# Kernel optimization log

Measured on AMD Instinct MI355X. Metric: run time of the kernel, lower is better.

The kernel has to match this reference:

```python
import jax, jax.numpy as jnp
import numpy as np
import math

BS, NPOS, D_IN = 8, 384, 512
H, D_OUT = 8, 512
DK = D_OUT // H  # 64


def setup_inputs() -> dict:
    key = jax.random.key(0)
    ks = jax.random.split(key, 13)
    s = 0.02
    return {
        "q": jax.random.normal(ks[0], (BS, NPOS, D_IN), jnp.float32),
        "k": jax.random.normal(ks[1], (BS, NPOS, D_IN), jnp.float32),
        "v": jax.random.normal(ks[2], (BS, NPOS, D_IN), jnp.float32),
        "rpos_k": jax.random.normal(ks[3], (NPOS, NPOS, H, DK), jnp.float32) * s,
        "rpos_v": jax.random.normal(ks[4], (NPOS, NPOS, H, DK), jnp.float32) * s,
        "Wq": jax.random.normal(ks[5], (D_IN, D_OUT), jnp.float32) * s,
        "bq": jnp.zeros((D_OUT,), jnp.float32),
        "Wk": jax.random.normal(ks[6], (D_IN, D_OUT), jnp.float32) * s,
        "bk": jnp.zeros((D_OUT,), jnp.float32),
        "Wv": jax.random.normal(ks[7], (D_IN, D_OUT), jnp.float32) * s,
        "bv": jnp.zeros((D_OUT,), jnp.float32),
        "Wo": jax.random.normal(ks[8], (D_OUT, D_OUT), jnp.float32) * s,
        "bo": jnp.zeros((D_OUT,), jnp.float32),
    }


def reference(q, k, v, rpos_k, rpos_v, Wq, bq, Wk, bk, Wv, bv, Wo, bo):
    # model_name = 'with_pe' path; mask=None; dropout in eval mode (no-op)
    bs = q.shape[0]
    inv_sqrt_dk = 1.0 / math.sqrt(DK)

    qh = (q @ Wq + bq).reshape(bs, -1, H, DK).transpose(0, 2, 1, 3)  # bs,h,n,dk
    kh = (k @ Wk + bk).reshape(bs, -1, H, DK).transpose(0, 2, 1, 3)
    original_v = v @ Wv + bv                                          # bs,n,d_out
    vh = original_v.reshape(bs, -1, H, DK).transpose(0, 2, 1, 3)

    # standard content-content scores
    std_scores = jnp.einsum('bhnd,bhmd->bhnm', qh, kh) * inv_sqrt_dk
    # relative-position scores: q_n . rpos_k[n, m, h] -- computed inline,
    # no bs-broadcast materialization of rpos_k
    pos_scores = jnp.einsum('bhnd,nmhd->bhnm', qh, rpos_k) * inv_sqrt_dk

    scores = jax.nn.softmax(std_scores + pos_scores, axis=-1)
    # NOTE: original code divides the attention output by sqrt(d_k) again
    attn_out = jnp.einsum('bhnm,bhmd->bhnd', scores, vh) * inv_sqrt_dk

    concat = attn_out.transpose(0, 2, 1, 3).reshape(bs, -1, D_OUT)
    output = concat @ Wo + bo
    return (original_v, output)
```

## Files before the change

kernel.cpp:

```cpp
#include <hip/hip_runtime.h>

#define NPOS 384
#define DMODEL 512
#define NH 8
#define DK 64
#define BS 8
#define MROWS (BS * NPOS)
#define SROW (NPOS * NPOS)

typedef __attribute__((ext_vector_type(8))) short bf16x8;
typedef __attribute__((ext_vector_type(4))) float f32x4;

__device__ __forceinline__ unsigned short f2bf(float x) {
  unsigned int u = __float_as_uint(x);
  return (unsigned short)((u + 0x7fffu + ((u >> 16) & 1u)) >> 16);
}
__device__ __forceinline__ unsigned int pk2(float lo, float hi) {
  unsigned int ul = __float_as_uint(lo), uh = __float_as_uint(hi);
  ul = (ul + 0x7fffu + ((ul >> 16) & 1u)) >> 16;
  uh = (uh + 0x7fffu + ((uh >> 16) & 1u)) & 0xffff0000u;
  return ul | uh;
}
__device__ __forceinline__ bf16x8 pack8(float4 a, float4 b) {
  union { uint4 u; bf16x8 v; } cv;
  cv.u = make_uint4(pk2(a.x, a.y), pk2(a.z, a.w), pk2(b.x, b.y), pk2(b.z, b.w));
  return cv.v;
}

__global__ __launch_bounds__(256) void convert_all(
    const float* __restrict__ qin, const float* __restrict__ kin,
    const float* __restrict__ vin,
    const float* __restrict__ Wq, const float* __restrict__ Wk,
    const float* __restrict__ Wv, const float* __restrict__ Wo,
    unsigned short* __restrict__ qkvb, unsigned short* __restrict__ wt) {
  const int z = blockIdx.y;
  const int t = threadIdx.x;
  if (z < 3) {
    const float* src = z == 0 ? qin : z == 1 ? kin : vin;
    unsigned short* dst = qkvb + (size_t)z * MROWS * DMODEL;
    const size_t i = ((size_t)blockIdx.x * 256 + t) * 8;
    float4 a = *(const float4*)&src[i];
    float4 b = *(const float4*)&src[i + 4];
    union { uint4 u; bf16x8 v; } cv;
    cv.u = make_uint4(pk2(a.x, a.y), pk2(a.z, a.w), pk2(b.x, b.y), pk2(b.z, b.w));
    *(uint4*)&dst[i] = cv.u;
    return;
  }
  if (blockIdx.x >= 64) return;
  __shared__ float s[64][68];
  const int w = z - 3;
  const float* W = w == 0 ? Wq : w == 1 ? Wk : w == 2 ? Wv : Wo;
  unsigned short* out = wt + (size_t)w * DMODEL * DMODEL;
  const int k0 = (blockIdx.x & 7) * 64, n0 = (blockIdx.x >> 3) * 64;
#pragma unroll
  for (int i = 0; i < 4; ++i) {
    int f = t + i * 256;
    int kr = f >> 4, q4 = f & 15;
    *(float4*)&s[kr][q4 * 4] = *(const float4*)&W[(size_t)(k0 + kr) * DMODEL + n0 + q4 * 4];
  }
  __syncthreads();
#pragma unroll
  for (int i = 0; i < 2; ++i) {
    int slot = t + i * 256;
    int n = slot >> 3, kq = slot & 7;
    unsigned int p[4];
#pragma unroll
    for (int j = 0; j < 4; ++j)
      p[j] = pk2(s[kq * 8 + j * 2][n], s[kq * 8 + j * 2 + 1][n]);
    *(uint4*)&out[(size_t)(n0 + n) * DMODEL + k0 + kq * 8] = make_uint4(p[0], p[1], p[2], p[3]);
  }
}

__global__ __launch_bounds__(256) void proj_qkv(
    const unsigned short* __restrict__ qkvb,
    const unsigned short* __restrict__ wt,
    const float* __restrict__ bq, const float* __restrict__ bk, const float* __restrict__ bv,
    unsigned short* __restrict__ qhb, unsigned short* __restrict__ khb,
    float* __restrict__ origv, unsigned short* __restrict__ vhT) {
  __shared__ unsigned short As[64][72];
  __shared__ unsigned short Bs[64][72];
  const int z = blockIdx.z;
  const unsigned short* A = qkvb + (size_t)z * MROWS * DMODEL;
  const unsigned short* Wt = wt + (size_t)z * DMODEL * DMODEL;
  const float* bias = z == 0 ? bq : z == 1 ? bk : bv;
  const int m0 = blockIdx.x * 64, n0 = blockIdx.y * 64;
  const int t = threadIdx.x, lane = t & 63, w = t >> 6;
  const int wr = w >> 1, wc = w & 1;
  const int l15 = lane & 15, l4 = lane >> 4;
  f32x4 acc[2][2] = {};
  for (int kt = 0; kt < 8; ++kt) {
    const int k0 = kt * 64;
#pragma unroll
    for (int i = 0; i < 2; ++i) {
      int s = t + i * 256;
      int row = s >> 3, kq = s & 7;
      *(uint4*)&As[row][kq * 8] = *(const uint4*)&A[(size_t)(m0 + row) * DMODEL + k0 + kq * 8];
      *(uint4*)&Bs[row][kq * 8] = *(const uint4*)&Wt[(size_t)(n0 + row) * DMODEL + k0 + kq * 8];
    }
    __syncthreads();
    bf16x8 af[2][2], bfr[2][2];
#pragma unroll
    for (int mf = 0; mf < 2; ++mf)
#pragma unroll
      for (int ks = 0; ks < 2; ++ks)
        af[mf][ks] = *(const bf16x8*)&As[wr * 32 + mf * 16 + l15][ks * 32 + l4 * 8];
#pragma unroll
    for (int nf = 0; nf < 2; ++nf)
#pragma unroll
      for (int ks = 0; ks < 2; ++ks)
        bfr[nf][ks] = *(const bf16x8*)&Bs[wc * 32 + nf * 16 + l15][ks * 32 + l4 * 8];
#pragma unroll
    for (int mf = 0; mf < 2; ++mf)
#pragma unroll
      for (int nf = 0; nf < 2; ++nf)
#pragma unroll
        for (int ks = 0; ks < 2; ++ks)
          acc[mf][nf] = __builtin_amdgcn_mfma_f32_16x16x32_bf16(af[mf][ks], bfr[nf][ks],
                                                                acc[mf][nf], 0, 0, 0);
    __syncthreads();
  }
#pragma unroll
  for (int mf = 0; mf < 2; ++mf)
#pragma unroll
    for (int nf = 0; nf < 2; ++nf) {
      const int row0 = m0 + wr * 32 + mf * 16 + l4 * 4;
      const int col = n0 + wc * 32 + nf * 16 + l15;
      const float bi = bias[col];
      if (z == 0) {
#pragma unroll
        for (int i = 0; i < 4; ++i)
          qhb[(size_t)(row0 + i) * DMODEL + col] = f2bf((acc[mf][nf][i] + bi) * 0.125f);
      } else if (z == 1) {
#pragma unroll
        for (int i = 0; i < 4; ++i)
          khb[(size_t)(row0 + i) * DMODEL + col] = f2bf(acc[mf][nf][i] + bi);
      } else {
        const int b = row0 / NPOS, n = row0 - b * NPOS;
        const int h = col >> 6, d = col & 63;
        float vals[4];
#pragma unroll
        for (int i = 0; i < 4; ++i) {
          vals[i] = acc[mf][nf][i] + bi;
          origv[(size_t)(row0 + i) * DMODEL + col] = vals[i];
        }
        ushort4 pk;
        pk.x = f2bf(vals[0]); pk.y = f2bf(vals[1]);
        pk.z = f2bf(vals[2]); pk.w = f2bf(vals[3]);
        *(ushort4*)&vhT[((size_t)((b * NH + h) * DK + d)) * NPOS + n] = pk;
      }
    }
}

__global__ __launch_bounds__(256) void scores_nt(
    const unsigned short* __restrict__ qhb, const unsigned short* __restrict__ khb,
    float* __restrict__ scores) {
  __shared__ unsigned short As[128][72];
  __shared__ unsigned short Bs[128][72];
  const int z = blockIdx.z, b = z >> 3, h = z & 7;
  const unsigned short* Ag = qhb + (size_t)b * NPOS * DMODEL + h * DK;
  const unsigned short* Bg = khb + (size_t)b * NPOS * DMODEL + h * DK;
  const int n0 = blockIdx.x * 128, m0 = blockIdx.y * 128;
  const int t = threadIdx.x, lane = t & 63, w = t >> 6;
  const int wr = w >> 1, wc = w & 1;
  const int l15 = lane & 15, l4 = lane >> 4;
#pragma unroll
  for (int i = 0; i < 4; ++i) {
    int s = t + i * 256;
    int row = s >> 3, kq = s & 7;
    *(uint4*)&As[row][kq * 8] = *(const uint4*)&Ag[(size_t)(n0 + row) * DMODEL + kq * 8];
    *(uint4*)&Bs[row][kq * 8] = *(const uint4*)&Bg[(size_t)(m0 + row) * DMODEL + kq * 8];
  }
  __syncthreads();
  f32x4 acc[4][4] = {};
  bf16x8 af[4][2], bfr[4][2];
#pragma unroll
  for (int mf = 0; mf < 4; ++mf)
#pragma unroll
    for (int ks = 0; ks < 2; ++ks)
      af[mf][ks] = *(const bf16x8*)&As[wr * 64 + mf * 16 + l15][ks * 32 + l4 * 8];
#pragma unroll
  for (int nf = 0; nf < 4; ++nf)
#pragma unroll
    for (int ks = 0; ks < 2; ++ks)
      bfr[nf][ks] = *(const bf16x8*)&Bs[wc * 64 + nf * 16 + l15][ks * 32 + l4 * 8];
#pragma unroll
  for (int mf = 0; mf < 4; ++mf)
#pragma unroll
    for (int nf = 0; nf < 4; ++nf)
#pragma unroll
      for (int ks = 0; ks < 2; ++ks)
        acc[mf][nf] = __builtin_amdgcn_mfma_f32_16x16x32_bf16(af[mf][ks], bfr[nf][ks],
                                                              acc[mf][nf], 0, 0, 0);
  float* C = scores + (size_t)z * SROW;
#pragma unroll
  for (int mf = 0; mf < 4; ++mf)
#pragma unroll
    for (int nf = 0; nf < 4; ++nf) {
      int rown = n0 + wr * 64 + mf * 16 + l4 * 4;
      int colm = m0 + wc * 64 + nf * 16 + l15;
#pragma unroll
      for (int i = 0; i < 4; ++i)
        C[(size_t)(rown + i) * NPOS + colm] = acc[mf][nf][i];
    }
}

__global__ __launch_bounds__(256) void pos_sm(
    const unsigned short* __restrict__ qhb,
    const float* __restrict__ rk,
    float* __restrict__ scores) {
  __shared__ float Pf[8][392];
  const int h = blockIdx.x;
  const int n = blockIdx.y;
  const int t = threadIdx.x, lane = t & 63, w = t >> 6;
  const int l15 = lane & 15, l4 = lane >> 4;
  const int bcol = l15 & 7;
  const unsigned short* qp = qhb + ((size_t)bcol * NPOS + n) * DMODEL + h * DK;
  const bf16x8 bfr0 = *(const bf16x8*)&qp[l4 * 8];
  const bf16x8 bfr1 = *(const bf16x8*)&qp[32 + l4 * 8];
#pragma unroll
  for (int mt = 0; mt < 6; ++mt) {
    const int m0 = w * 96 + mt * 16;
    const float* rkrow = rk + ((size_t)n * NPOS + m0 + l15) * (NH * DK) + h * DK;
    f32x4 acc = {};
    const float4 ra = *(const float4*)&rkrow[l4 * 8];
    const float4 rb = *(const float4*)&rkrow[l4 * 8 + 4];
    acc = __builtin_amdgcn_mfma_f32_16x16x32_bf16(pack8(ra, rb), bfr0, acc, 0, 0, 0);
    const float4 rc = *(const float4*)&rkrow[32 + l4 * 8];
    const float4 rd = *(const float4*)&rkrow[32 + l4 * 8 + 4];
    acc = __builtin_amdgcn_mfma_f32_16x16x32_bf16(pack8(rc, rd), bfr1, acc, 0, 0, 0);
    if (l15 < 8) {
#pragma unroll
      for (int i = 0; i < 4; ++i) Pf[l15][m0 + l4 * 4 + i] = acc[i];
    }
  }
  __syncthreads();
#pragma unroll
  for (int rr = 0; rr < 2; ++rr) {
    const int b = w * 2 + rr;
    float* srow = scores + ((size_t)(b * NH + h) * NPOS + n) * NPOS;
    unsigned short* prow = (unsigned short*)srow;
    float v[6];
    float mx = -1e30f;
#pragma unroll
    for (int j = 0; j < 6; ++j) {
      v[j] = srow[j * 64 + lane] + Pf[b][j * 64 + lane];
      mx = fmaxf(mx, v[j]);
    }
#pragma unroll
    for (int o = 32; o; o >>= 1) mx = fmaxf(mx, __shfl_xor(mx, o, 64));
    float sum = 0.f;
#pragma unroll
    for (int j = 0; j < 6; ++j) {
      v[j] = __expf(v[j] - mx);
      sum += v[j];
    }
#pragma unroll
    for (int o = 32; o; o >>= 1) sum += __shfl_xor(sum, o, 64);
    const float inv = 0.125f / sum;
#pragma unroll
    for (int j = 0; j < 6; ++j) prow[j * 64 + lane] = f2bf(v[j] * inv);
  }
}

__global__ __launch_bounds__(256) void pv_nt(
    const unsigned short* __restrict__ Pbase,
    const unsigned short* __restrict__ vhT,
    unsigned short* __restrict__ attb) {
  __shared__ unsigned short As[64][72];
  __shared__ unsigned short Bs[64][72];
  const int z = blockIdx.z, b = z >> 3, h = z & 7;
  const int n0 = blockIdx.x * 64;
  const unsigned short* Ag = Pbase + ((size_t)(z * NPOS + n0)) * 768;
  const unsigned short* Bg = vhT + (size_t)z * DK * NPOS;
  const int t = threadIdx.x, lane = t & 63, w = t >> 6;
  const int wr = w >> 1, wc = w & 1;
  const int l15 = lane & 15, l4 = lane >> 4;
  f32x4 acc[2][2] = {};
  for (int kt = 0; kt < 6; ++kt) {
    const int k0 = kt * 64;
#pragma unroll
    for (int i = 0; i < 2; ++i) {
      int s = t + i * 256;
      int row = s >> 3, kq = s & 7;
      *(uint4*)&As[row][kq * 8] = *(const uint4*)&Ag[(size_t)row * 768 + k0 + kq * 8];
      *(uint4*)&Bs[row][kq * 8] = *(const uint4*)&Bg[(size_t)row * NPOS + k0 + kq * 8];
    }
    __syncthreads();
    bf16x8 af[2][2], bfr[2][2];
#pragma unroll
    for (int mf = 0; mf < 2; ++mf)
#pragma unroll
      for (int ks = 0; ks < 2; ++ks)
        af[mf][ks] = *(const bf16x8*)&As[wr * 32 + mf * 16 + l15][ks * 32 + l4 * 8];
#pragma unroll
    for (int nf = 0; nf < 2; ++nf)
#pragma unroll
      for (int ks = 0; ks < 2; ++ks)
        bfr[nf][ks] = *(const bf16x8*)&Bs[wc * 32 + nf * 16 + l15][ks * 32 + l4 * 8];
#pragma unroll
    for (int mf = 0; mf < 2; ++mf)
#pragma unroll
      for (int nf = 0; nf < 2; ++nf)
#pragma unroll
        for (int ks = 0; ks < 2; ++ks)
          acc[mf][nf] = __builtin_amdgcn_mfma_f32_16x16x32_bf16(af[mf][ks], bfr[nf][ks],
                                                                acc[mf][nf], 0, 0, 0);
    __syncthreads();
  }
#pragma unroll
  for (int mf = 0; mf < 2; ++mf)
#pragma unroll
    for (int nf = 0; nf < 2; ++nf) {
      const int n = n0 + wr * 32 + mf * 16 + l4 * 4;
      const int d = wc * 32 + nf * 16 + l15;
#pragma unroll
      for (int i = 0; i < 4; ++i)
        attb[(size_t)(b * NPOS + n + i) * DMODEL + h * DK + d] = f2bf(acc[mf][nf][i]);
    }
}

__global__ __launch_bounds__(256) void proj_o(
    const unsigned short* __restrict__ attb, const unsigned short* __restrict__ WtO,
    const float* __restrict__ bo, float* __restrict__ outp) {
  __shared__ unsigned short As[64][72];
  __shared__ unsigned short Bs[64][72];
  const int m0 = blockIdx.x * 64, n0 = blockIdx.y * 64;
  const int t = threadIdx.x, lane = t & 63, w = t >> 6;
  const int wr = w >> 1, wc = w & 1;
  const int l15 = lane & 15, l4 = lane >> 4;
  f32x4 acc[2][2] = {};
  for (int kt = 0; kt < 8; ++kt) {
    const int k0 = kt * 64;
#pragma unroll
    for (int i = 0; i < 2; ++i) {
      int s = t + i * 256;
      int row = s >> 3, kq = s & 7;
      *(uint4*)&As[row][kq * 8] = *(const uint4*)&attb[(size_t)(m0 + row) * DMODEL + k0 + kq * 8];
      *(uint4*)&Bs[row][kq * 8] = *(const uint4*)&WtO[(size_t)(n0 + row) * DMODEL + k0 + kq * 8];
    }
    __syncthreads();
    bf16x8 af[2][2], bfr[2][2];
#pragma unroll
    for (int mf = 0; mf < 2; ++mf)
#pragma unroll
      for (int ks = 0; ks < 2; ++ks)
        af[mf][ks] = *(const bf16x8*)&As[wr * 32 + mf * 16 + l15][ks * 32 + l4 * 8];
#pragma unroll
    for (int nf = 0; nf < 2; ++nf)
#pragma unroll
      for (int ks = 0; ks < 2; ++ks)
        bfr[nf][ks] = *(const bf16x8*)&Bs[wc * 32 + nf * 16 + l15][ks * 32 + l4 * 8];
#pragma unroll
    for (int mf = 0; mf < 2; ++mf)
#pragma unroll
      for (int nf = 0; nf < 2; ++nf)
#pragma unroll
        for (int ks = 0; ks < 2; ++ks)
          acc[mf][nf] = __builtin_amdgcn_mfma_f32_16x16x32_bf16(af[mf][ks], bfr[nf][ks],
                                                                acc[mf][nf], 0, 0, 0);
    __syncthreads();
  }
#pragma unroll
  for (int mf = 0; mf < 2; ++mf)
#pragma unroll
    for (int nf = 0; nf < 2; ++nf) {
      const int row0 = m0 + wr * 32 + mf * 16 + l4 * 4;
      const int col = n0 + wc * 32 + nf * 16 + l15;
      const float bi = bo[col];
#pragma unroll
      for (int i = 0; i < 4; ++i)
        outp[(size_t)(row0 + i) * DMODEL + col] = acc[mf][nf][i] + bi;
    }
}

extern "C" void kernel_launch(void* const* d_in, const int* in_sizes, int n_in,
                              void* d_out, int out_size, void* d_ws, size_t ws_size,
                              hipStream_t stream) {
  const float* q  = (const float*)d_in[0];
  const float* k  = (const float*)d_in[1];
  const float* v  = (const float*)d_in[2];
  const float* rk = (const float*)d_in[3];
  const float* Wq = (const float*)d_in[5];
  const float* bq = (const float*)d_in[6];
  const float* Wk = (const float*)d_in[7];
  const float* bk = (const float*)d_in[8];
  const float* Wv = (const float*)d_in[9];
  const float* bv = (const float*)d_in[10];
  const float* Wo = (const float*)d_in[11];
  const float* bo = (const float*)d_in[12];

  const size_t TOK = (size_t)MROWS * DMODEL;
  unsigned short* wt   = (unsigned short*)d_ws;
  unsigned short* qhb  = wt + 4 * DMODEL * DMODEL;
  unsigned short* khb  = qhb + TOK;
  unsigned short* vhT  = khb + TOK;
  unsigned short* attb = vhT + TOK;
  float* scores = (float*)(attb + TOK);
  unsigned short* qkvb = (unsigned short*)scores;
  float* origv = (float*)d_out;
  float* outp = origv + TOK;

  dim3 blk(256);

  convert_all<<<dim3(768, 7), blk, 0, stream>>>(q, k, v, Wq, Wk, Wv, Wo, qkvb, wt);
  proj_qkv<<<dim3(48, 8, 3), blk, 0, stream>>>(qkvb, wt, bq, bk, bv,
                                               qhb, khb, origv, vhT);
  scores_nt<<<dim3(3, 3, 64), blk, 0, stream>>>(qhb, khb, scores);
  pos_sm<<<dim3(8, 384), blk, 0, stream>>>(qhb, rk, scores);
  pv_nt<<<dim3(6, 1, 64), blk, 0, stream>>>((const unsigned short*)scores, vhT, attb);
  proj_o<<<dim3(48, 8), blk, 0, stream>>>(attb, wt + 3 * DMODEL * DMODEL, bo, outp);
}
```

Before: 134.4 us.

## Fuse content-content QK scores into the positional-score softmax kernel

Removes the separate scores_nt GEMM and its fp32 score buffer. The pos_sm kernel now computes q·k for each batch with MFMA (keeping only the diagonal lane per batch) and accumulates the positional term into the same accumulator before softmax, writing bf16 probabilities into a compact NPOS-stride buffer. This drops one launch and a full fp32 score write and read. In exchange it does 8x redundant MFMA work (only one of 16 columns kept per batch), reloads K rows from global memory per query row, and serializes the mt loop.

```diff
diff --git a/kernel.cpp b/kernel.cpp
--- a/kernel.cpp
+++ b/kernel.cpp
@@ -6,7 +6,6 @@
 #define DK 64
 #define BS 8
 #define MROWS (BS * NPOS)
-#define SROW (NPOS * NPOS)
 
 typedef __attribute__((ext_vector_type(8))) short bf16x8;
 typedef __attribute__((ext_vector_type(4))) float f32x4;
@@ -151,99 +150,56 @@
     }
 }
 
-__global__ __launch_bounds__(256) void scores_nt(
-    const unsigned short* __restrict__ qhb, const unsigned short* __restrict__ khb,
-    float* __restrict__ scores) {
-  __shared__ unsigned short As[128][72];
-  __shared__ unsigned short Bs[128][72];
-  const int z = blockIdx.z, b = z >> 3, h = z & 7;
-  const unsigned short* Ag = qhb + (size_t)b * NPOS * DMODEL + h * DK;
-  const unsigned short* Bg = khb + (size_t)b * NPOS * DMODEL + h * DK;
-  const int n0 = blockIdx.x * 128, m0 = blockIdx.y * 128;
-  const int t = threadIdx.x, lane = t & 63, w = t >> 6;
-  const int wr = w >> 1, wc = w & 1;
-  const int l15 = lane & 15, l4 = lane >> 4;
-#pragma unroll
-  for (int i = 0; i < 4; ++i) {
-    int s = t + i * 256;
-    int row = s >> 3, kq = s & 7;
-    *(uint4*)&As[row][kq * 8] = *(const uint4*)&Ag[(size_t)(n0 + row) * DMODEL + kq * 8];
-    *(uint4*)&Bs[row][kq * 8] = *(const uint4*)&Bg[(size_t)(m0 + row) * DMODEL + kq * 8];
-  }
-  __syncthreads();
-  f32x4 acc[4][4] = {};
-  bf16x8 af[4][2], bfr[4][2];
-#pragma unroll
-  for (int mf = 0; mf < 4; ++mf)
-#pragma unroll
-    for (int ks = 0; ks < 2; ++ks)
-      af[mf][ks] = *(const bf16x8*)&As[wr * 64 + mf * 16 + l15][ks * 32 + l4 * 8];
-#pragma unroll
-  for (int nf = 0; nf < 4; ++nf)
-#pragma unroll
-    for (int ks = 0; ks < 2; ++ks)
-      bfr[nf][ks] = *(const bf16x8*)&Bs[wc * 64 + nf * 16 + l15][ks * 32 + l4 * 8];
-#pragma unroll
-  for (int mf = 0; mf < 4; ++mf)
-#pragma unroll
-    for (int nf = 0; nf < 4; ++nf)
-#pragma unroll
-      for (int ks = 0; ks < 2; ++ks)
-        acc[mf][nf] = __builtin_amdgcn_mfma_f32_16x16x32_bf16(af[mf][ks], bfr[nf][ks],
-                                                              acc[mf][nf], 0, 0, 0);
-  float* C = scores + (size_t)z * SROW;
-#pragma unroll
-  for (int mf = 0; mf < 4; ++mf)
-#pragma unroll
-    for (int nf = 0; nf < 4; ++nf) {
-      int rown = n0 + wr * 64 + mf * 16 + l4 * 4;
-      int colm = m0 + wc * 64 + nf * 16 + l15;
-#pragma unroll
-      for (int i = 0; i < 4; ++i)
-        C[(size_t)(rown + i) * NPOS + colm] = acc[mf][nf][i];
-    }
-}
-
 __global__ __launch_bounds__(256) void pos_sm(
     const unsigned short* __restrict__ qhb,
+    const unsigned short* __restrict__ khb,
     const float* __restrict__ rk,
-    float* __restrict__ scores) {
+    unsigned short* __restrict__ P) {
   __shared__ float Pf[8][392];
   const int h = blockIdx.x;
   const int n = blockIdx.y;
   const int t = threadIdx.x, lane = t & 63, w = t >> 6;
   const int l15 = lane & 15, l4 = lane >> 4;
   const int bcol = l15 & 7;
-  const unsigned short* qp = qhb + ((size_t)bcol * NPOS + n) * DMODEL + h * DK;
-  const bf16x8 bfr0 = *(const bf16x8*)&qp[l4 * 8];
-  const bf16x8 bfr1 = *(const bf16x8*)&qp[32 + l4 * 8];
-#pragma unroll
+  const unsigned short* qpb = qhb + ((size_t)bcol * NPOS + n) * DMODEL + h * DK;
+  const bf16x8 pb0 = *(const bf16x8*)&qpb[l4 * 8];
+  const bf16x8 pb1 = *(const bf16x8*)&qpb[32 + l4 * 8];
+#pragma unroll 1
   for (int mt = 0; mt < 6; ++mt) {
     const int m0 = w * 96 + mt * 16;
     const float* rkrow = rk + ((size_t)n * NPOS + m0 + l15) * (NH * DK) + h * DK;
-    f32x4 acc = {};
     const float4 ra = *(const float4*)&rkrow[l4 * 8];
     const float4 rb = *(const float4*)&rkrow[l4 * 8 + 4];
-    acc = __builtin_amdgcn_mfma_f32_16x16x32_bf16(pack8(ra, rb), bfr0, acc, 0, 0, 0);
     const float4 rc = *(const float4*)&rkrow[32 + l4 * 8];
     const float4 rd = *(const float4*)&rkrow[32 + l4 * 8 + 4];
-    acc = __builtin_amdgcn_mfma_f32_16x16x32_bf16(pack8(rc, rd), bfr1, acc, 0, 0, 0);
-    if (l15 < 8) {
-#pragma unroll
-      for (int i = 0; i < 4; ++i) Pf[l15][m0 + l4 * 4 + i] = acc[i];
-    }
+    f32x4 keep = {};
+#pragma unroll
+    for (int b = 0; b < 8; ++b) {
+      const unsigned short* kbase = khb + ((size_t)b * NPOS + m0 + l15) * DMODEL + h * DK;
+      const unsigned short* qb = qhb + ((size_t)b * NPOS + n) * DMODEL + h * DK;
+      f32x4 acc = {};
+      acc = __builtin_amdgcn_mfma_f32_16x16x32_bf16(
+          *(const bf16x8*)&kbase[l4 * 8], *(const bf16x8*)&qb[l4 * 8], acc, 0, 0, 0);
+      acc = __builtin_amdgcn_mfma_f32_16x16x32_bf16(
+          *(const bf16x8*)&kbase[32 + l4 * 8], *(const bf16x8*)&qb[32 + l4 * 8], acc, 0, 0, 0);
+      if (l15 == b) {
+        keep[0] += acc[0]; keep[1] += acc[1]; keep[2] += acc[2]; keep[3] += acc[3];
+      }
+    }
+    keep = __builtin_amdgcn_mfma_f32_16x16x32_bf16(pack8(ra, rb), pb0, keep, 0, 0, 0);
+    keep = __builtin_amdgcn_mfma_f32_16x16x32_bf16(pack8(rc, rd), pb1, keep, 0, 0, 0);
+    if (l15 < 8)
+      *(float4*)&Pf[l15][m0 + l4 * 4] = make_float4(keep[0], keep[1], keep[2], keep[3]);
   }
   __syncthreads();
 #pragma unroll
   for (int rr = 0; rr < 2; ++rr) {
     const int b = w * 2 + rr;
-    float* srow = scores + ((size_t)(b * NH + h) * NPOS + n) * NPOS;
-    unsigned short* prow = (unsigned short*)srow;
     float v[6];
     float mx = -1e30f;
 #pragma unroll
     for (int j = 0; j < 6; ++j) {
-      v[j] = srow[j * 64 + lane] + Pf[b][j * 64 + lane];
+      v[j] = Pf[b][j * 64 + lane];
       mx = fmaxf(mx, v[j]);
     }
 #pragma unroll
@@ -257,20 +213,21 @@
 #pragma unroll
     for (int o = 32; o; o >>= 1) sum += __shfl_xor(sum, o, 64);
     const float inv = 0.125f / sum;
+    unsigned short* prow = P + ((size_t)(b * NH + h) * NPOS + n) * NPOS;
 #pragma unroll
     for (int j = 0; j < 6; ++j) prow[j * 64 + lane] = f2bf(v[j] * inv);
   }
 }
 
 __global__ __launch_bounds__(256) void pv_nt(
-    const unsigned short* __restrict__ Pbase,
+    const unsigned short* __restrict__ P,
     const unsigned short* __restrict__ vhT,
     unsigned short* __restrict__ attb) {
   __shared__ unsigned short As[64][72];
   __shared__ unsigned short Bs[64][72];
   const int z = blockIdx.z, b = z >> 3, h = z & 7;
   const int n0 = blockIdx.x * 64;
-  const unsigned short* Ag = Pbase + ((size_t)(z * NPOS + n0)) * 768;
+  const unsigned short* Ag = P + ((size_t)z * NPOS + n0) * NPOS;
   const unsigned short* Bg = vhT + (size_t)z * DK * NPOS;
   const int t = threadIdx.x, lane = t & 63, w = t >> 6;
   const int wr = w >> 1, wc = w & 1;
@@ -282,7 +239,7 @@
     for (int i = 0; i < 2; ++i) {
       int s = t + i * 256;
       int row = s >> 3, kq = s & 7;
-      *(uint4*)&As[row][kq * 8] = *(const uint4*)&Ag[(size_t)row * 768 + k0 + kq * 8];
+      *(uint4*)&As[row][kq * 8] = *(const uint4*)&Ag[(size_t)row * NPOS + k0 + kq * 8];
       *(uint4*)&Bs[row][kq * 8] = *(const uint4*)&Bg[(size_t)row * NPOS + k0 + kq * 8];
     }
     __syncthreads();
@@ -311,11 +268,11 @@
   for (int mf = 0; mf < 2; ++mf)
 #pragma unroll
     for (int nf = 0; nf < 2; ++nf) {
-      const int n = n0 + wr * 32 + mf * 16 + l4 * 4;
+      const int nn = n0 + wr * 32 + mf * 16 + l4 * 4;
       const int d = wc * 32 + nf * 16 + l15;
 #pragma unroll
       for (int i = 0; i < 4; ++i)
-        attb[(size_t)(b * NPOS + n + i) * DMODEL + h * DK + d] = f2bf(acc[mf][nf][i]);
+        attb[(size_t)(b * NPOS + nn + i) * DMODEL + h * DK + d] = f2bf(acc[mf][nf][i]);
     }
 }
 
@@ -395,8 +352,8 @@
   unsigned short* khb  = qhb + TOK;
   unsigned short* vhT  = khb + TOK;
   unsigned short* attb = vhT + TOK;
-  float* scores = (float*)(attb + TOK);
-  unsigned short* qkvb = (unsigned short*)scores;
+  unsigned short* P    = attb + TOK;
+  unsigned short* qkvb = P;
   float* origv = (float*)d_out;
   float* outp = origv + TOK;
 
@@ -405,8 +362,7 @@
   convert_all<<<dim3(768, 7), blk, 0, stream>>>(q, k, v, Wq, Wk, Wv, Wo, qkvb, wt);
   proj_qkv<<<dim3(48, 8, 3), blk, 0, stream>>>(qkvb, wt, bq, bk, bv,
                                                qhb, khb, origv, vhT);
-  scores_nt<<<dim3(3, 3, 64), blk, 0, stream>>>(qhb, khb, scores);
-  pos_sm<<<dim3(8, 384), blk, 0, stream>>>(qhb, rk, scores);
-  pv_nt<<<dim3(6, 1, 64), blk, 0, stream>>>((const unsigned short*)scores, vhT, attb);
+  pos_sm<<<dim3(8, 384), blk, 0, stream>>>(qhb, khb, rk, P);
+  pv_nt<<<dim3(6, 1, 64), blk, 0, stream>>>(P, vhT, attb);
   proj_o<<<dim3(48, 8), blk, 0, stream>>>(attb, wt + 3 * DMODEL * DMODEL, bo, outp);
 }
```

Result: slower. 257.2 us (+91.4%).

## Store raw scores in bf16, split S/P buffers, shrink PV tile to 32 rows

Applied to the files above, without the earlier changes.

The score matrix is now written as bf16 instead of fp32, halving the write and read traffic between scores_nt and pos_sm. Softmax results go to a separate dense P buffer instead of in-place with stride 768. The PV kernel uses 32-row tiles, doubling its grid to 768 blocks for better occupancy. The cost is extra rounding of pre-softmax logits to bf16, which loses some precision.

```diff
diff --git a/kernel.cpp b/kernel.cpp
--- a/kernel.cpp
+++ b/kernel.cpp
@@ -6,7 +6,6 @@
 #define DK 64
 #define BS 8
 #define MROWS (BS * NPOS)
-#define SROW (NPOS * NPOS)
 
 typedef __attribute__((ext_vector_type(8))) short bf16x8;
 typedef __attribute__((ext_vector_type(4))) float f32x4;
@@ -14,6 +13,9 @@
 __device__ __forceinline__ unsigned short f2bf(float x) {
   unsigned int u = __float_as_uint(x);
   return (unsigned short)((u + 0x7fffu + ((u >> 16) & 1u)) >> 16);
+}
+__device__ __forceinline__ float bf2f(unsigned short x) {
+  return __uint_as_float((unsigned int)x << 16);
 }
 __device__ __forceinline__ unsigned int pk2(float lo, float hi) {
   unsigned int ul = __float_as_uint(lo), uh = __float_as_uint(hi);
@@ -153,7 +155,7 @@
 
 __global__ __launch_bounds__(256) void scores_nt(
     const unsigned short* __restrict__ qhb, const unsigned short* __restrict__ khb,
-    float* __restrict__ scores) {
+    unsigned short* __restrict__ S) {
   __shared__ unsigned short As[128][72];
   __shared__ unsigned short Bs[128][72];
   const int z = blockIdx.z, b = z >> 3, h = z & 7;
@@ -191,7 +193,7 @@
       for (int ks = 0; ks < 2; ++ks)
         acc[mf][nf] = __builtin_amdgcn_mfma_f32_16x16x32_bf16(af[mf][ks], bfr[nf][ks],
                                                               acc[mf][nf], 0, 0, 0);
-  float* C = scores + (size_t)z * SROW;
+  unsigned short* C = S + (size_t)z * NPOS * NPOS;
 #pragma unroll
   for (int mf = 0; mf < 4; ++mf)
 #pragma unroll
@@ -200,23 +202,24 @@
       int colm = m0 + wc * 64 + nf * 16 + l15;
 #pragma unroll
       for (int i = 0; i < 4; ++i)
-        C[(size_t)(rown + i) * NPOS + colm] = acc[mf][nf][i];
+        C[(size_t)(rown + i) * NPOS + colm] = f2bf(acc[mf][nf][i]);
     }
 }
 
 __global__ __launch_bounds__(256) void pos_sm(
     const unsigned short* __restrict__ qhb,
+    const unsigned short* __restrict__ S,
     const float* __restrict__ rk,
-    float* __restrict__ scores) {
+    unsigned short* __restrict__ P) {
   __shared__ float Pf[8][392];
   const int h = blockIdx.x;
   const int n = blockIdx.y;
   const int t = threadIdx.x, lane = t & 63, w = t >> 6;
   const int l15 = lane & 15, l4 = lane >> 4;
   const int bcol = l15 & 7;
-  const unsigned short* qp = qhb + ((size_t)bcol * NPOS + n) * DMODEL + h * DK;
-  const bf16x8 bfr0 = *(const bf16x8*)&qp[l4 * 8];
-  const bf16x8 bfr1 = *(const bf16x8*)&qp[32 + l4 * 8];
+  const unsigned short* qpb = qhb + ((size_t)bcol * NPOS + n) * DMODEL + h * DK;
+  const bf16x8 pb0 = *(const bf16x8*)&qpb[l4 * 8];
+  const bf16x8 pb1 = *(const bf16x8*)&qpb[32 + l4 * 8];
 #pragma unroll
   for (int mt = 0; mt < 6; ++mt) {
     const int m0 = w * 96 + mt * 16;
@@ -224,10 +227,10 @@
     f32x4 acc = {};
     const float4 ra = *(const float4*)&rkrow[l4 * 8];
     const float4 rb = *(const float4*)&rkrow[l4 * 8 + 4];
-    acc = __builtin_amdgcn_mfma_f32_16x16x32_bf16(pack8(ra, rb), bfr0, acc, 0, 0, 0);
+    acc = __builtin_amdgcn_mfma_f32_16x16x32_bf16(pack8(ra, rb), pb0, acc, 0, 0, 0);
     const float4 rc = *(const float4*)&rkrow[32 + l4 * 8];
     const float4 rd = *(const float4*)&rkrow[32 + l4 * 8 + 4];
-    acc = __builtin_amdgcn_mfma_f32_16x16x32_bf16(pack8(rc, rd), bfr1, acc, 0, 0, 0);
+    acc = __builtin_amdgcn_mfma_f32_16x16x32_bf16(pack8(rc, rd), pb1, acc, 0, 0, 0);
     if (l15 < 8) {
 #pragma unroll
       for (int i = 0; i < 4; ++i) Pf[l15][m0 + l4 * 4 + i] = acc[i];
@@ -237,13 +240,13 @@
 #pragma unroll
   for (int rr = 0; rr < 2; ++rr) {
     const int b = w * 2 + rr;
-    float* srow = scores + ((size_t)(b * NH + h) * NPOS + n) * NPOS;
-    unsigned short* prow = (unsigned short*)srow;
+    const unsigned short* srow = S + ((size_t)(b * NH + h) * NPOS + n) * NPOS;
+    unsigned short* prow = P + ((size_t)(b * NH + h) * NPOS + n) * NPOS;
     float v[6];
     float mx = -1e30f;
 #pragma unroll
     for (int j = 0; j < 6; ++j) {
-      v[j] = srow[j * 64 + lane] + Pf[b][j * 64 + lane];
+      v[j] = bf2f(srow[j * 64 + lane]) + Pf[b][j * 64 + lane];
       mx = fmaxf(mx, v[j]);
     }
 #pragma unroll
@@ -263,60 +266,57 @@
 }
 
 __global__ __launch_bounds__(256) void pv_nt(
-    const unsigned short* __restrict__ Pbase,
+    const unsigned short* __restrict__ P,
     const unsigned short* __restrict__ vhT,
     unsigned short* __restrict__ attb) {
-  __shared__ unsigned short As[64][72];
+  __shared__ unsigned short As[32][72];
   __shared__ unsigned short Bs[64][72];
-  const int z = blockIdx.z, b = z >> 3, h = z & 7;
-  const int n0 = blockIdx.x * 64;
-  const unsigned short* Ag = Pbase + ((size_t)(z * NPOS + n0)) * 768;
+  const int z = blockIdx.y, b = z >> 3, h = z & 7;
+  const int n0 = blockIdx.x * 32;
+  const unsigned short* Ag = P + ((size_t)z * NPOS + n0) * NPOS;
   const unsigned short* Bg = vhT + (size_t)z * DK * NPOS;
   const int t = threadIdx.x, lane = t & 63, w = t >> 6;
   const int wr = w >> 1, wc = w & 1;
   const int l15 = lane & 15, l4 = lane >> 4;
-  f32x4 acc[2][2] = {};
+  f32x4 acc[2] = {};
   for (int kt = 0; kt < 6; ++kt) {
     const int k0 = kt * 64;
-#pragma unroll
-    for (int i = 0; i < 2; ++i) {
-      int s = t + i * 256;
-      int row = s >> 3, kq = s & 7;
-      *(uint4*)&As[row][kq * 8] = *(const uint4*)&Ag[(size_t)row * 768 + k0 + kq * 8];
-      *(uint4*)&Bs[row][kq * 8] = *(const uint4*)&Bg[(size_t)row * NPOS + k0 + kq * 8];
-    }
-    __syncthreads();
-    bf16x8 af[2][2], bfr[2][2];
-#pragma unroll
-    for (int mf = 0; mf < 2; ++mf)
-#pragma unroll
-      for (int ks = 0; ks < 2; ++ks)
-        af[mf][ks] = *(const bf16x8*)&As[wr * 32 + mf * 16 + l15][ks * 32 + l4 * 8];
+    {
+      int rowA = t >> 3, kqA = t & 7;
+      *(uint4*)&As[rowA][kqA * 8] = *(const uint4*)&Ag[(size_t)rowA * NPOS + k0 + kqA * 8];
+#pragma unroll
+      for (int i = 0; i < 2; ++i) {
+        int s = t + i * 256;
+        int row = s >> 3, kq = s & 7;
+        *(uint4*)&Bs[row][kq * 8] = *(const uint4*)&Bg[(size_t)row * NPOS + k0 + kq * 8];
+      }
+    }
+    __syncthreads();
+    bf16x8 af[2], bfr[2][2];
+#pragma unroll
+    for (int ks = 0; ks < 2; ++ks)
+      af[ks] = *(const bf16x8*)&As[wr * 16 + l15][ks * 32 + l4 * 8];
 #pragma unroll
     for (int nf = 0; nf < 2; ++nf)
 #pragma unroll
       for (int ks = 0; ks < 2; ++ks)
         bfr[nf][ks] = *(const bf16x8*)&Bs[wc * 32 + nf * 16 + l15][ks * 32 + l4 * 8];
 #pragma unroll
-    for (int mf = 0; mf < 2; ++mf)
-#pragma unroll
-      for (int nf = 0; nf < 2; ++nf)
-#pragma unroll
-        for (int ks = 0; ks < 2; ++ks)
-          acc[mf][nf] = __builtin_amdgcn_mfma_f32_16x16x32_bf16(af[mf][ks], bfr[nf][ks],
-                                                                acc[mf][nf], 0, 0, 0);
-    __syncthreads();
-  }
-#pragma unroll
-  for (int mf = 0; mf < 2; ++mf)
-#pragma unroll
-    for (int nf = 0; nf < 2; ++nf) {
-      const int n = n0 + wr * 32 + mf * 16 + l4 * 4;
-      const int d = wc * 32 + nf * 16 + l15;
-#pragma unroll
-      for (int i = 0; i < 4; ++i)
-        attb[(size_t)(b * NPOS + n + i) * DMODEL + h * DK + d] = f2bf(acc[mf][nf][i]);
-    }
+    for (int nf = 0; nf < 2; ++nf)
+#pragma unroll
+      for (int ks = 0; ks < 2; ++ks)
+        acc[nf] = __builtin_amdgcn_mfma_f32_16x16x32_bf16(af[ks], bfr[nf][ks],
+                                                          acc[nf], 0, 0, 0);
+    __syncthreads();
+  }
+#pragma unroll
+  for (int nf = 0; nf < 2; ++nf) {
+    const int nn = n0 + wr * 16 + l4 * 4;
+    const int d = wc * 32 + nf * 16 + l15;
+#pragma unroll
+    for (int i = 0; i < 4; ++i)
+      attb[(size_t)(b * NPOS + nn + i) * DMODEL + h * DK + d] = f2bf(acc[nf][i]);
+  }
 }
 
 __global__ __launch_bounds__(256) void proj_o(
@@ -390,13 +390,15 @@
   const float* bo = (const float*)d_in[12];
 
   const size_t TOK = (size_t)MROWS * DMODEL;
+  const size_t SEL = (size_t)BS * NH * NPOS * NPOS;
   unsigned short* wt   = (unsigned short*)d_ws;
   unsigned short* qhb  = wt + 4 * DMODEL * DMODEL;
   unsigned short* khb  = qhb + TOK;
   unsigned short* vhT  = khb + TOK;
   unsigned short* attb = vhT + TOK;
-  float* scores = (float*)(attb + TOK);
-  unsigned short* qkvb = (unsigned short*)scores;
+  unsigned short* S    = attb + TOK;
+  unsigned short* P    = S + SEL;
+  unsigned short* qkvb = P;
   float* origv = (float*)d_out;
   float* outp = origv + TOK;
 
@@ -405,8 +407,8 @@
   convert_all<<<dim3(768, 7), blk, 0, stream>>>(q, k, v, Wq, Wk, Wv, Wo, qkvb, wt);
   proj_qkv<<<dim3(48, 8, 3), blk, 0, stream>>>(qkvb, wt, bq, bk, bv,
                                                qhb, khb, origv, vhT);
-  scores_nt<<<dim3(3, 3, 64), blk, 0, stream>>>(qhb, khb, scores);
-  pos_sm<<<dim3(8, 384), blk, 0, stream>>>(qhb, rk, scores);
-  pv_nt<<<dim3(6, 1, 64), blk, 0, stream>>>((const unsigned short*)scores, vhT, attb);
+  scores_nt<<<dim3(3, 3, 64), blk, 0, stream>>>(qhb, khb, S);
+  pos_sm<<<dim3(8, 384), blk, 0, stream>>>(qhb, S, rk, P);
+  pv_nt<<<dim3(12, 64), blk, 0, stream>>>(P, vhT, attb);
   proj_o<<<dim3(48, 8), blk, 0, stream>>>(attb, wt + 3 * DMODEL * DMODEL, bo, outp);
 }
```

Result: faster. 129.8 us (-3.5%).
